# Kernel optimization log

Hardware: AMD Instinct MI355X
Metric: run time of the kernel (lower is better)

## Reference

```python
import jax, jax.numpy as jnp
import numpy as np

NUM_HEADS = 16
NEG_BIG = 1e9


def setup_inputs() -> dict:
    key = jax.random.key(0)
    k1, k2, k3 = jax.random.split(key, 3)
    B, T, D = 2, 2048, 1024
    x = jax.random.normal(k1, (B, T, D), dtype=jnp.float32)
    W_attn = jax.random.normal(k2, (D, 3 * D), dtype=jnp.float32) * 0.02
    b_attn = jnp.zeros((3 * D,), dtype=jnp.float32)
    W_proj = jax.random.normal(k3, (D, D), dtype=jnp.float32) * 0.02
    b_proj = jnp.zeros((D,), dtype=jnp.float32)
    return {"x": x, "W_attn": W_attn, "b_attn": b_attn, "W_proj": W_proj, "b_proj": b_proj}


def reference(x, W_attn, b_attn, W_proj, b_proj):
    B, T, D = x.shape
    H = NUM_HEADS
    dh = D // H
    # qkv projection (GPT-style Conv1D == linear)
    qkv = jnp.einsum('btd,de->bte', x, W_attn) + b_attn  # [B,T,3D]
    q, k, v = jnp.split(qkv, 3, axis=-1)
    # split heads -> [B,H,T,dh]
    q = q.reshape(B, T, H, dh).transpose(0, 2, 1, 3)
    k = k.reshape(B, T, H, dh).transpose(0, 2, 1, 3)
    v = v.reshape(B, T, H, dh).transpose(0, 2, 1, 3)
    # scores [B,H,T,T]; scale=True divides by sqrt(head_dim)
    w = jnp.einsum('bhqd,bhkd->bhqk', q, k) / jnp.sqrt(jnp.float32(dh))
    # causal mask: multiplicative tril then large additive negative, as in source
    mask = jnp.tril(jnp.ones((T, T), dtype=w.dtype))[None, None, :, :]
    w = w * mask - NEG_BIG * (1.0 - mask)
    p = jax.nn.softmax(w, axis=-1)  # attn dropout = identity (eval mode)
    out = jnp.einsum('bhqk,bhkd->bhqd', p, v)  # [B,H,T,dh]
    out = out.transpose(0, 2, 1, 3).reshape(B, T, D)  # merge heads
    out = jnp.einsum('btd,de->bte', out, W_proj) + b_proj  # residual dropout = identity
    return out
```

## Files before the change

### kernel.cpp

```cpp
#include <hip/hip_runtime.h>

typedef unsigned short u16;
typedef unsigned u32;
typedef __bf16 bf16x8 __attribute__((ext_vector_type(8)));
typedef __bf16 bf16x2 __attribute__((ext_vector_type(2)));
typedef float f32x4 __attribute__((ext_vector_type(4)));
typedef u16 u16x4 __attribute__((ext_vector_type(4)));
typedef u32 u32x2 __attribute__((ext_vector_type(2)));
typedef u32 u32x4 __attribute__((ext_vector_type(4)));

__device__ __forceinline__ u16 f2bf(float f) {
  u32 u = __float_as_uint(f);
  u += 0x7fffu + ((u >> 16) & 1u);
  return (u16)(u >> 16);
}

__device__ __forceinline__ u32 pk2(float a, float b) {
#if __has_builtin(__builtin_amdgcn_cvt_pk_bf16_f32)
  bf16x2 r = __builtin_amdgcn_cvt_pk_bf16_f32(a, b);
  return __builtin_bit_cast(u32, r);
#else
  return (u32)f2bf(a) | ((u32)f2bf(b) << 16);
#endif
}

__device__ __forceinline__ float fast_exp2(float x) {
  return __builtin_amdgcn_exp2f(x);
}

__device__ __forceinline__ void gload16(const u16* g, u16* l) {
  __builtin_amdgcn_global_load_lds((__attribute__((address_space(1))) void*)g,
                                   (__attribute__((address_space(3))) void*)l,
                                   16, 0, 0);
}

__global__ __launch_bounds__(256) void cvt_f32_bf16(const float* __restrict__ in,
                                                    u16* __restrict__ out, int n4) {
  int i = blockIdx.x * 256 + threadIdx.x;
  if (i >= n4) return;
  float4 v = ((const float4*)in)[i];
  u16x4 o = { f2bf(v.x), f2bf(v.y), f2bf(v.z), f2bf(v.w) };
  ((u16x4*)out)[i] = o;
}

__global__ __launch_bounds__(256) void transpose_cvt(const float* __restrict__ in,
                                                     u16* __restrict__ out, int R, int C) {
  __shared__ float tile[32][33];
  int c0 = blockIdx.x * 32, r0 = blockIdx.y * 32;
  int tx = threadIdx.x & 31, ty = threadIdx.x >> 5;
#pragma unroll
  for (int i = 0; i < 32; i += 8)
    tile[ty + i][tx] = in[(size_t)(r0 + ty + i) * C + c0 + tx];
  __syncthreads();
#pragma unroll
  for (int i = 0; i < 32; i += 8)
    out[(size_t)(c0 + ty + i) * R + r0 + tx] = f2bf(tile[tx][ty + i]);
}

template <int EPI>
__global__ __launch_bounds__(256) void gemm_bt(const u16* __restrict__ A,
                                               const u16* __restrict__ Bt, int K,
                                               const float* __restrict__ bias,
                                               float* __restrict__ outF,
                                               u16* __restrict__ qb, u16* __restrict__ kb,
                                               u16* __restrict__ vtb) {
  __shared__ __align__(16) u16 As[128 * 32];
  __shared__ __align__(16) u16 Bs[128 * 32];
  const int tid = threadIdx.x;
  const int w = tid >> 6, lane = tid & 63, quad = lane >> 4, l16 = lane & 15;
  const int wm = w >> 1, wn = w & 1;
  const int tm = blockIdx.y * 128, tn = blockIdx.x * 128;

  f32x4 acc[4][4] = {};

  const int ra = lane >> 2;
  const int ca = (lane & 3) * 8;
  const u16* gA0 = A + (size_t)(tm + w * 16 + ra) * K + ca;
  const u16* gA1 = A + (size_t)(tm + (w + 4) * 16 + ra) * K + ca;
  const u16* gB0 = Bt + (size_t)(tn + w * 16 + ra) * K + ca;
  const u16* gB1 = Bt + (size_t)(tn + (w + 4) * 16 + ra) * K + ca;
  u16* lA0 = &As[(w * 16) * 32];
  u16* lA1 = &As[((w + 4) * 16) * 32];
  u16* lB0 = &Bs[(w * 16) * 32];
  u16* lB1 = &Bs[((w + 4) * 16) * 32];

  for (int k0 = 0; k0 < K; k0 += 32) {
    gload16(gA0 + k0, lA0);
    gload16(gA1 + k0, lA1);
    gload16(gB0 + k0, lB0);
    gload16(gB1 + k0, lB1);
    __syncthreads();
    bf16x8 af[4], bfr[4];
#pragma unroll
    for (int mt = 0; mt < 4; ++mt)
      af[mt] = *(const bf16x8*)&As[(wm * 64 + mt * 16 + l16) * 32 + quad * 8];
#pragma unroll
    for (int nt = 0; nt < 4; ++nt)
      bfr[nt] = *(const bf16x8*)&Bs[(wn * 64 + nt * 16 + l16) * 32 + quad * 8];
#pragma unroll
    for (int mt = 0; mt < 4; ++mt)
#pragma unroll
      for (int nt = 0; nt < 4; ++nt)
        acc[mt][nt] = __builtin_amdgcn_mfma_f32_16x16x32_bf16(af[mt], bfr[nt], acc[mt][nt], 0, 0, 0);
    __syncthreads();
  }

#pragma unroll
  for (int mt = 0; mt < 4; ++mt) {
#pragma unroll
    for (int nt = 0; nt < 4; ++nt) {
      const int row0 = tm + wm * 64 + mt * 16 + quad * 4;
      const int col = tn + wn * 64 + nt * 16 + l16;
      float v4[4];
#pragma unroll
      for (int r = 0; r < 4; ++r) v4[r] = acc[mt][nt][r] + bias[col];
      if (EPI == 0) {
        int which = col >> 10, d = col & 1023, hh = d >> 6, dd = d & 63;
        int b = row0 >> 11, t = row0 & 2047;
        int bh = (b << 4) + hh;
        if (which == 0) {
#pragma unroll
          for (int r = 0; r < 4; ++r)
            qb[((size_t)bh * 2048 + t + r) * 64 + dd] = f2bf(v4[r] * 0.18033688f);
        } else if (which == 1) {
#pragma unroll
          for (int r = 0; r < 4; ++r)
            kb[((size_t)bh * 2048 + t + r) * 64 + dd] = f2bf(v4[r]);
        } else {
          u16x4 pk = { f2bf(v4[0]), f2bf(v4[1]), f2bf(v4[2]), f2bf(v4[3]) };
          *(u16x4*)(vtb + ((size_t)bh * 64 + dd) * 2048 + t) = pk;
        }
      } else {
#pragma unroll
        for (int r = 0; r < 4; ++r)
          outF[(size_t)(row0 + r) * 1024 + col] = v4[r];
      }
    }
  }
}

__global__ __launch_bounds__(256) void gemm_bt_64(const u16* __restrict__ A,
                                                  const u16* __restrict__ Bt, int K,
                                                  const float* __restrict__ bias,
                                                  float* __restrict__ outF) {
  __shared__ __align__(16) u16 As[64 * 32];
  __shared__ __align__(16) u16 Bs[128 * 32];
  const int tid = threadIdx.x;
  const int w = tid >> 6, lane = tid & 63, quad = lane >> 4, l16 = lane & 15;
  const int wm = w >> 1, wn = w & 1;
  const int tm = blockIdx.y * 64, tn = blockIdx.x * 128;

  f32x4 acc[2][4] = {};

  const int ra = lane >> 2;
  const int ca = (lane & 3) * 8;
  const u16* gA0 = A + (size_t)(tm + w * 16 + ra) * K + ca;
  const u16* gB0 = Bt + (size_t)(tn + w * 16 + ra) * K + ca;
  const u16* gB1 = Bt + (size_t)(tn + (w + 4) * 16 + ra) * K + ca;
  u16* lA0 = &As[(w * 16) * 32];
  u16* lB0 = &Bs[(w * 16) * 32];
  u16* lB1 = &Bs[((w + 4) * 16) * 32];

  for (int k0 = 0; k0 < K; k0 += 32) {
    gload16(gA0 + k0, lA0);
    gload16(gB0 + k0, lB0);
    gload16(gB1 + k0, lB1);
    __syncthreads();
    bf16x8 af[2], bfr[4];
#pragma unroll
    for (int mt = 0; mt < 2; ++mt)
      af[mt] = *(const bf16x8*)&As[(wm * 32 + mt * 16 + l16) * 32 + quad * 8];
#pragma unroll
    for (int nt = 0; nt < 4; ++nt)
      bfr[nt] = *(const bf16x8*)&Bs[(wn * 64 + nt * 16 + l16) * 32 + quad * 8];
#pragma unroll
    for (int mt = 0; mt < 2; ++mt)
#pragma unroll
      for (int nt = 0; nt < 4; ++nt)
        acc[mt][nt] = __builtin_amdgcn_mfma_f32_16x16x32_bf16(af[mt], bfr[nt], acc[mt][nt], 0, 0, 0);
    __syncthreads();
  }

#pragma unroll
  for (int mt = 0; mt < 2; ++mt) {
#pragma unroll
    for (int nt = 0; nt < 4; ++nt) {
      const int row0 = tm + wm * 32 + mt * 16 + quad * 4;
      const int col = tn + wn * 64 + nt * 16 + l16;
#pragma unroll
      for (int r = 0; r < 4; ++r)
        outF[(size_t)(row0 + r) * 1024 + col] = acc[mt][nt][r] + bias[col];
    }
  }
}

__global__ __launch_bounds__(256) void flash_attn(const u16* __restrict__ qb,
                                                  const u16* __restrict__ kb,
                                                  const u16* __restrict__ vtb,
                                                  u16* __restrict__ ao) {
  const int T = 2048;
  const int tid = threadIdx.x;
  const int w = tid >> 6, lane = tid & 63;
  const int quad = lane >> 4, l16 = lane & 15;
  const int bx = blockIdx.x;
  const int bh = bx & 31;
  const int g0 = bx >> 5;
  const int G = (g0 & 24) | (((g0 >> 3) & 1) ? (7 - (g0 & 7)) : (g0 & 7));
  const int b = bh >> 4, h = bh & 15;
  const int ro = w * 16 + l16;
  const int qrow = G * 64 + ro;
  const size_t kvbase = (size_t)bh * T * 64;
  const int nkt = G + 1;

  __shared__ __align__(16) u16 Ks[64][72];
  __shared__ __align__(16) u16 Vs[64][72];
  __shared__ __align__(16) u16 Ps[4][16][72];

  bf16x8 q0 = *(const bf16x8*)(qb + kvbase + (size_t)qrow * 64 + quad * 8);
  bf16x8 q1 = *(const bf16x8*)(qb + kvbase + (size_t)qrow * 64 + 32 + quad * 8);

  bf16x8 ones;
#pragma unroll
  for (int i = 0; i < 8; ++i) ones[i] = (__bf16)1.0f;

  f32x4 o[4] = {};
  f32x4 o_lp = {};

  const int tok = tid >> 2, c4 = (tid & 3) * 16;
  const u16* kg = kb + kvbase + (size_t)tok * 64 + c4;
  const u16* vg = vtb + (size_t)(bh * 64 + tok) * 2048 + c4;

  {
    u32x4 a0 = *(const u32x4*)(kg);
    u32x4 a1 = *(const u32x4*)(kg + 8);
    u32x4 b0 = *(const u32x4*)(vg);
    u32x4 b1 = *(const u32x4*)(vg + 8);
    *(u32x4*)&Ks[tok][c4] = a0;  *(u32x4*)&Ks[tok][c4 + 8] = a1;
    *(u32x4*)&Vs[tok][c4] = b0;  *(u32x4*)&Vs[tok][c4 + 8] = b1;
  }
  __syncthreads();

  u32x4 sk0, sk1, sv0, sv1;

  for (int kt = 0; kt < nkt; ++kt) {
    const bool more = (kt + 1 < nkt);
    if (more) {
      const int kb2 = (kt + 1) * 64;
      sk0 = *(const u32x4*)(kg + (size_t)kb2 * 64);
      sk1 = *(const u32x4*)(kg + (size_t)kb2 * 64 + 8);
      sv0 = *(const u32x4*)(vg + kb2);
      sv1 = *(const u32x4*)(vg + kb2 + 8);
    }

    f32x4 z[4];
#pragma unroll
    for (int st = 0; st < 4; ++st) {
      bf16x8 kf0 = *(const bf16x8*)&Ks[st * 16 + l16][quad * 8];
      bf16x8 kf1 = *(const bf16x8*)&Ks[st * 16 + l16][32 + quad * 8];
      f32x4 zz = {};
      zz = __builtin_amdgcn_mfma_f32_16x16x32_bf16(kf0, q0, zz, 0, 0, 0);
      zz = __builtin_amdgcn_mfma_f32_16x16x32_bf16(kf1, q1, zz, 0, 0, 0);
      z[st] = zz;
    }
    if (kt == nkt - 1) {
#pragma unroll
      for (int st = 0; st < 4; ++st)
#pragma unroll
        for (int r = 0; r < 4; ++r)
          if (st * 16 + quad * 4 + r > ro) z[st][r] = -1e30f;
    }
#pragma unroll
    for (int st = 0; st < 4; ++st) {
      float p0 = fast_exp2(z[st][0]), p1 = fast_exp2(z[st][1]);
      float p2 = fast_exp2(z[st][2]), p3 = fast_exp2(z[st][3]);
      u32x2 pw = { pk2(p0, p1), pk2(p2, p3) };
      *(u32x2*)&Ps[w][l16][st * 16 + quad * 4] = pw;
    }

    bf16x8 pf0 = *(const bf16x8*)&Ps[w][l16][quad * 8];
    bf16x8 pf1 = *(const bf16x8*)&Ps[w][l16][32 + quad * 8];
    o_lp = __builtin_amdgcn_mfma_f32_16x16x32_bf16(ones, pf0, o_lp, 0, 0, 0);
    o_lp = __builtin_amdgcn_mfma_f32_16x16x32_bf16(ones, pf1, o_lp, 0, 0, 0);
#pragma unroll
    for (int dt = 0; dt < 4; ++dt) {
      bf16x8 vf0 = *(const bf16x8*)&Vs[dt * 16 + l16][quad * 8];
      bf16x8 vf1 = *(const bf16x8*)&Vs[dt * 16 + l16][32 + quad * 8];
      o[dt] = __builtin_amdgcn_mfma_f32_16x16x32_bf16(vf0, pf0, o[dt], 0, 0, 0);
      o[dt] = __builtin_amdgcn_mfma_f32_16x16x32_bf16(vf1, pf1, o[dt], 0, 0, 0);
    }

    __syncthreads();
    if (more) {
      *(u32x4*)&Ks[tok][c4] = sk0;  *(u32x4*)&Ks[tok][c4 + 8] = sk1;
      *(u32x4*)&Vs[tok][c4] = sv0;  *(u32x4*)&Vs[tok][c4 + 8] = sv1;
    }
    __syncthreads();
  }

  float inv = 1.0f / o_lp[0];
  size_t obase = ((size_t)b * T + qrow) * 1024 + h * 64;
#pragma unroll
  for (int dt = 0; dt < 4; ++dt) {
    u16x4 ov = { f2bf(o[dt][0] * inv), f2bf(o[dt][1] * inv),
                 f2bf(o[dt][2] * inv), f2bf(o[dt][3] * inv) };
    *(u16x4*)(ao + obase + dt * 16 + quad * 4) = ov;
  }
}

extern "C" void kernel_launch(void* const* d_in, const int* in_sizes, int n_in,
                              void* d_out, int out_size, void* d_ws, size_t ws_size,
                              hipStream_t stream) {
  const float* x      = (const float*)d_in[0];
  const float* W_attn = (const float*)d_in[1];
  const float* b_attn = (const float*)d_in[2];
  const float* W_proj = (const float*)d_in[3];
  const float* b_proj = (const float*)d_in[4];
  float* out = (float*)d_out;

  if (ws_size < 50331648u) return;

  char* ws = (char*)d_ws;
  u16* xb  = (u16*)(ws);
  u16* wat = (u16*)(ws + 8388608u);
  u16* wpt = (u16*)(ws + 14680064u);
  u16* qb  = (u16*)(ws + 16777216u);
  u16* kb  = (u16*)(ws + 25165824u);
  u16* vtb = (u16*)(ws + 33554432u);
  u16* ao  = (u16*)(ws + 41943040u);

  cvt_f32_bf16<<<4096, 256, 0, stream>>>(x, xb, 4194304 / 4);
  transpose_cvt<<<dim3(96, 32), 256, 0, stream>>>(W_attn, wat, 1024, 3072);
  transpose_cvt<<<dim3(32, 32), 256, 0, stream>>>(W_proj, wpt, 1024, 1024);

  gemm_bt<0><<<dim3(24, 32), 256, 0, stream>>>(xb, wat, 1024, b_attn, nullptr, qb, kb, vtb);

  flash_attn<<<dim3(1024), 256, 0, stream>>>(qb, kb, vtb, ao);

  gemm_bt_64<<<dim3(8, 64), 256, 0, stream>>>(ao, wpt, 1024, b_proj, out);
}
```

Before: 187.7 us.

## Process 128 query rows per attention block to reuse each K/V tile twice

The flash attention block now covers 128 query rows instead of 64, with each wave handling two 16-row groups. Every K/V tile loaded into shared memory feeds twice as many MFMAs, which halves global K/V traffic and barrier overhead per query row. Waves whose rows lie entirely before a tile skip its compute under causal masking. The grid halves to 512 blocks, which lowers parallelism, raises register pressure, and can leave some waves idle during the diagonal tiles.

```diff
diff --git a/kernel.cpp b/kernel.cpp
--- a/kernel.cpp
+++ b/kernel.cpp
@@ -205,26 +205,30 @@
   const int bx = blockIdx.x;
   const int bh = bx & 31;
   const int g0 = bx >> 5;
-  const int G = (g0 & 24) | (((g0 >> 3) & 1) ? (7 - (g0 & 7)) : (g0 & 7));
+  const int G = (g0 & 8) | (((g0 >> 3) & 1) ? (7 - (g0 & 7)) : (g0 & 7));
   const int b = bh >> 4, h = bh & 15;
-  const int ro = w * 16 + l16;
-  const int qrow = G * 64 + ro;
+  const int rw = w * 32;
   const size_t kvbase = (size_t)bh * T * 64;
-  const int nkt = G + 1;
+  const int nkt = 2 * G + 2;
 
   __shared__ __align__(16) u16 Ks[64][72];
   __shared__ __align__(16) u16 Vs[64][72];
-  __shared__ __align__(16) u16 Ps[4][16][72];
-
-  bf16x8 q0 = *(const bf16x8*)(qb + kvbase + (size_t)qrow * 64 + quad * 8);
-  bf16x8 q1 = *(const bf16x8*)(qb + kvbase + (size_t)qrow * 64 + 32 + quad * 8);
+  __shared__ __align__(16) u16 Ps[4][32][72];
+
+  bf16x8 q[2][2];
+#pragma unroll
+  for (int g = 0; g < 2; ++g) {
+    const int qrow_g = G * 128 + rw + g * 16 + l16;
+    q[g][0] = *(const bf16x8*)(qb + kvbase + (size_t)qrow_g * 64 + quad * 8);
+    q[g][1] = *(const bf16x8*)(qb + kvbase + (size_t)qrow_g * 64 + 32 + quad * 8);
+  }
 
   bf16x8 ones;
 #pragma unroll
   for (int i = 0; i < 8; ++i) ones[i] = (__bf16)1.0f;
 
-  f32x4 o[4] = {};
-  f32x4 o_lp = {};
+  f32x4 o[2][4] = {};
+  f32x4 olp[2] = {};
 
   const int tok = tid >> 2, c4 = (tid & 3) * 16;
   const u16* kg = kb + kvbase + (size_t)tok * 64 + c4;
@@ -252,41 +256,61 @@
       sv1 = *(const u32x4*)(vg + kb2 + 8);
     }
 
-    f32x4 z[4];
-#pragma unroll
-    for (int st = 0; st < 4; ++st) {
-      bf16x8 kf0 = *(const bf16x8*)&Ks[st * 16 + l16][quad * 8];
-      bf16x8 kf1 = *(const bf16x8*)&Ks[st * 16 + l16][32 + quad * 8];
-      f32x4 zz = {};
-      zz = __builtin_amdgcn_mfma_f32_16x16x32_bf16(kf0, q0, zz, 0, 0, 0);
-      zz = __builtin_amdgcn_mfma_f32_16x16x32_bf16(kf1, q1, zz, 0, 0, 0);
-      z[st] = zz;
-    }
-    if (kt == nkt - 1) {
-#pragma unroll
-      for (int st = 0; st < 4; ++st)
-#pragma unroll
-        for (int r = 0; r < 4; ++r)
-          if (st * 16 + quad * 4 + r > ro) z[st][r] = -1e30f;
-    }
-#pragma unroll
-    for (int st = 0; st < 4; ++st) {
-      float p0 = fast_exp2(z[st][0]), p1 = fast_exp2(z[st][1]);
-      float p2 = fast_exp2(z[st][2]), p3 = fast_exp2(z[st][3]);
-      u32x2 pw = { pk2(p0, p1), pk2(p2, p3) };
-      *(u32x2*)&Ps[w][l16][st * 16 + quad * 4] = pw;
-    }
-
-    bf16x8 pf0 = *(const bf16x8*)&Ps[w][l16][quad * 8];
-    bf16x8 pf1 = *(const bf16x8*)&Ps[w][l16][32 + quad * 8];
-    o_lp = __builtin_amdgcn_mfma_f32_16x16x32_bf16(ones, pf0, o_lp, 0, 0, 0);
-    o_lp = __builtin_amdgcn_mfma_f32_16x16x32_bf16(ones, pf1, o_lp, 0, 0, 0);
-#pragma unroll
-    for (int dt = 0; dt < 4; ++dt) {
-      bf16x8 vf0 = *(const bf16x8*)&Vs[dt * 16 + l16][quad * 8];
-      bf16x8 vf1 = *(const bf16x8*)&Vs[dt * 16 + l16][32 + quad * 8];
-      o[dt] = __builtin_amdgcn_mfma_f32_16x16x32_bf16(vf0, pf0, o[dt], 0, 0, 0);
-      o[dt] = __builtin_amdgcn_mfma_f32_16x16x32_bf16(vf1, pf1, o[dt], 0, 0, 0);
+    const bool active = (kt * 64) <= (G * 128 + rw + 31);
+    if (active) {
+      f32x4 z[2][4];
+#pragma unroll
+      for (int st = 0; st < 4; ++st) {
+        bf16x8 kf0 = *(const bf16x8*)&Ks[st * 16 + l16][quad * 8];
+        bf16x8 kf1 = *(const bf16x8*)&Ks[st * 16 + l16][32 + quad * 8];
+#pragma unroll
+        for (int g = 0; g < 2; ++g) {
+          f32x4 zz = {};
+          zz = __builtin_amdgcn_mfma_f32_16x16x32_bf16(kf0, q[g][0], zz, 0, 0, 0);
+          zz = __builtin_amdgcn_mfma_f32_16x16x32_bf16(kf1, q[g][1], zz, 0, 0, 0);
+          z[g][st] = zz;
+        }
+      }
+      if (kt * 64 + 63 > G * 128 + rw) {
+        const int kb0 = kt * 64 - G * 128;
+#pragma unroll
+        for (int g = 0; g < 2; ++g) {
+          const int rg = rw + g * 16 + l16;
+#pragma unroll
+          for (int st = 0; st < 4; ++st)
+#pragma unroll
+            for (int r = 0; r < 4; ++r)
+              if (kb0 + st * 16 + quad * 4 + r > rg) z[g][st][r] = -1e30f;
+        }
+      }
+#pragma unroll
+      for (int g = 0; g < 2; ++g)
+#pragma unroll
+        for (int st = 0; st < 4; ++st) {
+          float p0 = fast_exp2(z[g][st][0]), p1 = fast_exp2(z[g][st][1]);
+          float p2 = fast_exp2(z[g][st][2]), p3 = fast_exp2(z[g][st][3]);
+          u32x2 pw = { pk2(p0, p1), pk2(p2, p3) };
+          *(u32x2*)&Ps[w][g * 16 + l16][st * 16 + quad * 4] = pw;
+        }
+
+      bf16x8 pf[2][2];
+#pragma unroll
+      for (int g = 0; g < 2; ++g) {
+        pf[g][0] = *(const bf16x8*)&Ps[w][g * 16 + l16][quad * 8];
+        pf[g][1] = *(const bf16x8*)&Ps[w][g * 16 + l16][32 + quad * 8];
+        olp[g] = __builtin_amdgcn_mfma_f32_16x16x32_bf16(ones, pf[g][0], olp[g], 0, 0, 0);
+        olp[g] = __builtin_amdgcn_mfma_f32_16x16x32_bf16(ones, pf[g][1], olp[g], 0, 0, 0);
+      }
+#pragma unroll
+      for (int dt = 0; dt < 4; ++dt) {
+        bf16x8 vf0 = *(const bf16x8*)&Vs[dt * 16 + l16][quad * 8];
+        bf16x8 vf1 = *(const bf16x8*)&Vs[dt * 16 + l16][32 + quad * 8];
+#pragma unroll
+        for (int g = 0; g < 2; ++g) {
+          o[g][dt] = __builtin_amdgcn_mfma_f32_16x16x32_bf16(vf0, pf[g][0], o[g][dt], 0, 0, 0);
+          o[g][dt] = __builtin_amdgcn_mfma_f32_16x16x32_bf16(vf1, pf[g][1], o[g][dt], 0, 0, 0);
+        }
+      }
     }
 
     __syncthreads();
@@ -297,13 +321,17 @@
     __syncthreads();
   }
 
-  float inv = 1.0f / o_lp[0];
-  size_t obase = ((size_t)b * T + qrow) * 1024 + h * 64;
-#pragma unroll
-  for (int dt = 0; dt < 4; ++dt) {
-    u16x4 ov = { f2bf(o[dt][0] * inv), f2bf(o[dt][1] * inv),
-                 f2bf(o[dt][2] * inv), f2bf(o[dt][3] * inv) };
-    *(u16x4*)(ao + obase + dt * 16 + quad * 4) = ov;
+#pragma unroll
+  for (int g = 0; g < 2; ++g) {
+    const float inv = 1.0f / olp[g][0];
+    const int qrow_g = G * 128 + rw + g * 16 + l16;
+    size_t obase = ((size_t)b * T + qrow_g) * 1024 + h * 64;
+#pragma unroll
+    for (int dt = 0; dt < 4; ++dt) {
+      u16x4 ov = { f2bf(o[g][dt][0] * inv), f2bf(o[g][dt][1] * inv),
+                   f2bf(o[g][dt][2] * inv), f2bf(o[g][dt][3] * inv) };
+      *(u16x4*)(ao + obase + dt * 16 + quad * 4) = ov;
+    }
   }
 }
 
@@ -334,7 +362,7 @@
 
   gemm_bt<0><<<dim3(24, 32), 256, 0, stream>>>(xb, wat, 1024, b_attn, nullptr, qb, kb, vtb);
 
-  flash_attn<<<dim3(1024), 256, 0, stream>>>(qb, kb, vtb, ao);
+  flash_attn<<<dim3(512), 256, 0, stream>>>(qb, kb, vtb, ao);
 
   gemm_bt_64<<<dim3(8, 64), 256, 0, stream>>>(ao, wpt, 1024, b_proj, out);
 }
```

Result: slower. 196.9 us (+4.9%).

## Pair mirrored causal query tiles per block to balance work and share K/V

Applied to the files above, without the earlier changes.

Each flash-attention block now handles two query tiles, g and 31-g, so every block does the same total causal work, and the K/V tiles it loads are reused for both. The grid shrinks from 1024 to 512 blocks. The aim is to remove causal load imbalance and halve K/V tile loads for the short tile. The cost is more registers and a larger P buffer in shared memory, which may lower occupancy, and fewer blocks in flight.

```diff
diff --git a/kernel.cpp b/kernel.cpp
--- a/kernel.cpp
+++ b/kernel.cpp
@@ -204,27 +204,30 @@
   const int quad = lane >> 4, l16 = lane & 15;
   const int bx = blockIdx.x;
   const int bh = bx & 31;
-  const int g0 = bx >> 5;
-  const int G = (g0 & 24) | (((g0 >> 3) & 1) ? (7 - (g0 & 7)) : (g0 & 7));
+  const int g = bx >> 5;
+  const int t2 = 31 - g;
   const int b = bh >> 4, h = bh & 15;
   const int ro = w * 16 + l16;
-  const int qrow = G * 64 + ro;
+  const int qrow1 = g * 64 + ro;
+  const int qrow2 = t2 * 64 + ro;
   const size_t kvbase = (size_t)bh * T * 64;
-  const int nkt = G + 1;
+  const int nkt = t2 + 1;
 
   __shared__ __align__(16) u16 Ks[64][72];
   __shared__ __align__(16) u16 Vs[64][72];
-  __shared__ __align__(16) u16 Ps[4][16][72];
-
-  bf16x8 q0 = *(const bf16x8*)(qb + kvbase + (size_t)qrow * 64 + quad * 8);
-  bf16x8 q1 = *(const bf16x8*)(qb + kvbase + (size_t)qrow * 64 + 32 + quad * 8);
+  __shared__ __align__(16) u16 Ps[4][32][72];
+
+  bf16x8 q1a = *(const bf16x8*)(qb + kvbase + (size_t)qrow1 * 64 + quad * 8);
+  bf16x8 q1b = *(const bf16x8*)(qb + kvbase + (size_t)qrow1 * 64 + 32 + quad * 8);
+  bf16x8 q2a = *(const bf16x8*)(qb + kvbase + (size_t)qrow2 * 64 + quad * 8);
+  bf16x8 q2b = *(const bf16x8*)(qb + kvbase + (size_t)qrow2 * 64 + 32 + quad * 8);
 
   bf16x8 ones;
 #pragma unroll
   for (int i = 0; i < 8; ++i) ones[i] = (__bf16)1.0f;
 
-  f32x4 o[4] = {};
-  f32x4 o_lp = {};
+  f32x4 o1[4] = {}, o2[4] = {};
+  f32x4 olp1 = {}, olp2 = {};
 
   const int tok = tid >> 2, c4 = (tid & 3) * 16;
   const u16* kg = kb + kvbase + (size_t)tok * 64 + c4;
@@ -252,41 +255,76 @@
       sv1 = *(const u32x4*)(vg + kb2 + 8);
     }
 
-    f32x4 z[4];
+    const bool grp1 = (kt <= g);
+
+    f32x4 z1[4], z2[4];
 #pragma unroll
     for (int st = 0; st < 4; ++st) {
       bf16x8 kf0 = *(const bf16x8*)&Ks[st * 16 + l16][quad * 8];
       bf16x8 kf1 = *(const bf16x8*)&Ks[st * 16 + l16][32 + quad * 8];
       f32x4 zz = {};
-      zz = __builtin_amdgcn_mfma_f32_16x16x32_bf16(kf0, q0, zz, 0, 0, 0);
-      zz = __builtin_amdgcn_mfma_f32_16x16x32_bf16(kf1, q1, zz, 0, 0, 0);
-      z[st] = zz;
+      zz = __builtin_amdgcn_mfma_f32_16x16x32_bf16(kf0, q2a, zz, 0, 0, 0);
+      zz = __builtin_amdgcn_mfma_f32_16x16x32_bf16(kf1, q2b, zz, 0, 0, 0);
+      z2[st] = zz;
+      if (grp1) {
+        f32x4 zy = {};
+        zy = __builtin_amdgcn_mfma_f32_16x16x32_bf16(kf0, q1a, zy, 0, 0, 0);
+        zy = __builtin_amdgcn_mfma_f32_16x16x32_bf16(kf1, q1b, zy, 0, 0, 0);
+        z1[st] = zy;
+      }
+    }
+    if (kt == g) {
+#pragma unroll
+      for (int st = 0; st < 4; ++st)
+#pragma unroll
+        for (int r = 0; r < 4; ++r)
+          if (st * 16 + quad * 4 + r > ro) z1[st][r] = -1e30f;
     }
     if (kt == nkt - 1) {
 #pragma unroll
       for (int st = 0; st < 4; ++st)
 #pragma unroll
         for (int r = 0; r < 4; ++r)
-          if (st * 16 + quad * 4 + r > ro) z[st][r] = -1e30f;
+          if (st * 16 + quad * 4 + r > ro) z2[st][r] = -1e30f;
     }
 #pragma unroll
     for (int st = 0; st < 4; ++st) {
-      float p0 = fast_exp2(z[st][0]), p1 = fast_exp2(z[st][1]);
-      float p2 = fast_exp2(z[st][2]), p3 = fast_exp2(z[st][3]);
+      float p0 = fast_exp2(z2[st][0]), p1 = fast_exp2(z2[st][1]);
+      float p2 = fast_exp2(z2[st][2]), p3 = fast_exp2(z2[st][3]);
       u32x2 pw = { pk2(p0, p1), pk2(p2, p3) };
-      *(u32x2*)&Ps[w][l16][st * 16 + quad * 4] = pw;
-    }
-
-    bf16x8 pf0 = *(const bf16x8*)&Ps[w][l16][quad * 8];
-    bf16x8 pf1 = *(const bf16x8*)&Ps[w][l16][32 + quad * 8];
-    o_lp = __builtin_amdgcn_mfma_f32_16x16x32_bf16(ones, pf0, o_lp, 0, 0, 0);
-    o_lp = __builtin_amdgcn_mfma_f32_16x16x32_bf16(ones, pf1, o_lp, 0, 0, 0);
+      *(u32x2*)&Ps[w][16 + l16][st * 16 + quad * 4] = pw;
+    }
+    if (grp1) {
+#pragma unroll
+      for (int st = 0; st < 4; ++st) {
+        float p0 = fast_exp2(z1[st][0]), p1 = fast_exp2(z1[st][1]);
+        float p2 = fast_exp2(z1[st][2]), p3 = fast_exp2(z1[st][3]);
+        u32x2 pw = { pk2(p0, p1), pk2(p2, p3) };
+        *(u32x2*)&Ps[w][l16][st * 16 + quad * 4] = pw;
+      }
+    }
+
+    bf16x8 pf2a = *(const bf16x8*)&Ps[w][16 + l16][quad * 8];
+    bf16x8 pf2b = *(const bf16x8*)&Ps[w][16 + l16][32 + quad * 8];
+    olp2 = __builtin_amdgcn_mfma_f32_16x16x32_bf16(ones, pf2a, olp2, 0, 0, 0);
+    olp2 = __builtin_amdgcn_mfma_f32_16x16x32_bf16(ones, pf2b, olp2, 0, 0, 0);
+    bf16x8 pf1a, pf1b;
+    if (grp1) {
+      pf1a = *(const bf16x8*)&Ps[w][l16][quad * 8];
+      pf1b = *(const bf16x8*)&Ps[w][l16][32 + quad * 8];
+      olp1 = __builtin_amdgcn_mfma_f32_16x16x32_bf16(ones, pf1a, olp1, 0, 0, 0);
+      olp1 = __builtin_amdgcn_mfma_f32_16x16x32_bf16(ones, pf1b, olp1, 0, 0, 0);
+    }
 #pragma unroll
     for (int dt = 0; dt < 4; ++dt) {
       bf16x8 vf0 = *(const bf16x8*)&Vs[dt * 16 + l16][quad * 8];
       bf16x8 vf1 = *(const bf16x8*)&Vs[dt * 16 + l16][32 + quad * 8];
-      o[dt] = __builtin_amdgcn_mfma_f32_16x16x32_bf16(vf0, pf0, o[dt], 0, 0, 0);
-      o[dt] = __builtin_amdgcn_mfma_f32_16x16x32_bf16(vf1, pf1, o[dt], 0, 0, 0);
+      o2[dt] = __builtin_amdgcn_mfma_f32_16x16x32_bf16(vf0, pf2a, o2[dt], 0, 0, 0);
+      o2[dt] = __builtin_amdgcn_mfma_f32_16x16x32_bf16(vf1, pf2b, o2[dt], 0, 0, 0);
+      if (grp1) {
+        o1[dt] = __builtin_amdgcn_mfma_f32_16x16x32_bf16(vf0, pf1a, o1[dt], 0, 0, 0);
+        o1[dt] = __builtin_amdgcn_mfma_f32_16x16x32_bf16(vf1, pf1b, o1[dt], 0, 0, 0);
+      }
     }
 
     __syncthreads();
@@ -297,13 +335,25 @@
     __syncthreads();
   }
 
-  float inv = 1.0f / o_lp[0];
-  size_t obase = ((size_t)b * T + qrow) * 1024 + h * 64;
-#pragma unroll
-  for (int dt = 0; dt < 4; ++dt) {
-    u16x4 ov = { f2bf(o[dt][0] * inv), f2bf(o[dt][1] * inv),
-                 f2bf(o[dt][2] * inv), f2bf(o[dt][3] * inv) };
-    *(u16x4*)(ao + obase + dt * 16 + quad * 4) = ov;
+  {
+    const float inv = 1.0f / olp1[0];
+    size_t obase = ((size_t)b * T + qrow1) * 1024 + h * 64;
+#pragma unroll
+    for (int dt = 0; dt < 4; ++dt) {
+      u16x4 ov = { f2bf(o1[dt][0] * inv), f2bf(o1[dt][1] * inv),
+                   f2bf(o1[dt][2] * inv), f2bf(o1[dt][3] * inv) };
+      *(u16x4*)(ao + obase + dt * 16 + quad * 4) = ov;
+    }
+  }
+  {
+    const float inv = 1.0f / olp2[0];
+    size_t obase = ((size_t)b * T + qrow2) * 1024 + h * 64;
+#pragma unroll
+    for (int dt = 0; dt < 4; ++dt) {
+      u16x4 ov = { f2bf(o2[dt][0] * inv), f2bf(o2[dt][1] * inv),
+                   f2bf(o2[dt][2] * inv), f2bf(o2[dt][3] * inv) };
+      *(u16x4*)(ao + obase + dt * 16 + quad * 4) = ov;
+    }
   }
 }
 
@@ -334,7 +384,7 @@
 
   gemm_bt<0><<<dim3(24, 32), 256, 0, stream>>>(xb, wat, 1024, b_attn, nullptr, qb, kb, vtb);
 
-  flash_attn<<<dim3(1024), 256, 0, stream>>>(qb, kb, vtb, ao);
+  flash_attn<<<dim3(512), 256, 0, stream>>>(qb, kb, vtb, ao);
 
   gemm_bt_64<<<dim3(8, 64), 256, 0, stream>>>(ao, wpt, 1024, b_proj, out);
 }
```

New measurement: 193.9 us. 1.03x slower.
